# Kernel tuning notes

Hardware: AMD Instinct MI355X
Metric: run time of the kernel (lower is better)

Reference implementation:

```python
import jax, jax.numpy as jnp
import numpy as np

N = 25600      # nodes
DEG = 16       # incoming edges per node
E = N * DEG    # 409600 edges
B = 8          # graphs in batch
F = 7          # node features
H = 300        # hidden_channels
L = 100        # latent_channels


def _mlp(h, W1, b1, W2, b2, W3, b3):
    h = jax.nn.relu(h @ W1 + b1)
    h = jax.nn.relu(h @ W2 + b2)
    return h @ W3 + b3


def _edge_layer(x, src, dst, params):
    # PyG MessagePassing(aggr='max'), flow source_to_target:
    # x_j = x[src] (edge_index[0]), x_i = x[dst] (edge_index[1])
    x_i = x[dst]
    x_j = x[src]
    m = _mlp(jnp.concatenate([x_i, x_j - x_i], axis=-1), *params)  # [E, out]
    # every node has >=1 incoming edge by construction, so no empty segments
    return jax.ops.segment_max(m, dst, num_segments=x.shape[0])


def setup_inputs() -> dict:
    key = jax.random.key(0)
    ks = jax.random.split(key, 24)
    x = jax.random.normal(ks[0], (N, F), jnp.float32)
    dst = jnp.repeat(jnp.arange(N, dtype=jnp.int32), DEG)          # every node covered
    src = jax.random.randint(ks[1], (E,), 0, N, dtype=jnp.int32)
    edge_index = jnp.stack([src, dst])                              # [2, E]
    batch = jnp.repeat(jnp.arange(B, dtype=jnp.int32), N // B)     # sorted graph ids

    def lin(k, i, o):
        return jax.random.normal(k, (i, o), jnp.float32) / jnp.sqrt(jnp.float32(i))

    def bias(k, o):
        return jax.random.normal(k, (o,), jnp.float32) * 0.01

    inp = dict(x=x, edge_index=edge_index, batch=batch)
    # layer 0 MLP: 2*F -> H -> H -> L
    inp.update(l0_W1=lin(ks[2], 2 * F, H), l0_b1=bias(ks[3], H),
               l0_W2=lin(ks[4], H, H),     l0_b2=bias(ks[5], H),
               l0_W3=lin(ks[6], H, L),     l0_b3=bias(ks[7], L))
    # layer 1 MLP: 2*L -> H -> H -> L
    inp.update(l1_W1=lin(ks[8], 2 * L, H), l1_b1=bias(ks[9], H),
               l1_W2=lin(ks[10], H, H),    l1_b2=bias(ks[11], H),
               l1_W3=lin(ks[12], H, L),    l1_b3=bias(ks[13], L))
    # final lin: 3*L -> L -> L -> 1
    inp.update(lin_W1=lin(ks[14], 3 * L, L), lin_b1=bias(ks[15], L),
               lin_W2=lin(ks[16], L, L),     lin_b2=bias(ks[17], L),
               lin_W3=lin(ks[18], L, 1),     lin_b3=bias(ks[19], 1))
    return inp


def reference(x, edge_index, batch,
              l0_W1, l0_b1, l0_W2, l0_b2, l0_W3, l0_b3,
              l1_W1, l1_b1, l1_W2, l1_b2, l1_W3, l1_b3,
              lin_W1, lin_b1, lin_W2, lin_b2, lin_W3, lin_b3):
    src, dst = edge_index[0], edge_index[1]
    h = _edge_layer(x, src, dst, (l0_W1, l0_b1, l0_W2, l0_b2, l0_W3, l0_b3))
    h = jax.nn.relu(h)
    h = _edge_layer(h, src, dst, (l1_W1, l1_b1, l1_W2, l1_b2, l1_W3, l1_b3))
    h = jax.nn.relu(h)                                              # [N, L]
    addp = jax.ops.segment_sum(h, batch, num_segments=B)
    cnt = jax.ops.segment_sum(jnp.ones((h.shape[0], 1), h.dtype), batch, num_segments=B)
    meanp = addp / cnt
    maxp = jax.ops.segment_max(h, batch, num_segments=B)
    pooled = jnp.concatenate([addp, meanp, maxp], axis=1)           # [B, 3L]
    return _mlp(pooled, lin_W1, lin_b1, lin_W2, lin_b2, lin_W3, lin_b3)  # [B, 1]
```

## Files before the change

kernel.cpp:

```cpp
#include <hip/hip_runtime.h>

#define NNODES 25600
#define DEG 16
#define BGRAPHS 8
#define NPG (NNODES / BGRAPHS)
#define FDIM 7
#define HDIM 300
#define LDIM 100
#define HP 320
#define UVW 640
#define NT1 20
#define KS1 10
#define NT2 7
#define KS2 10
#define H0W 128
#define SSTR 328

typedef __attribute__((ext_vector_type(8))) _Float16 half8;
typedef __attribute__((ext_vector_type(2))) _Float16 half2v;
typedef __attribute__((ext_vector_type(4))) float floatx4;

__device__ __forceinline__ unsigned short f2h(float f) {
    _Float16 h = (_Float16)f;
    return __builtin_bit_cast(unsigned short, h);
}

union UV4H { uint4 v; half2v h[4]; };

__device__ __forceinline__ unsigned short packB(const float* W, int Kreal, int Nreal,
                                                int KS, int rel)
{
    int j = rel & 7, lane = (rel >> 3) & 63, rem = rel >> 9;
    int ks = rem % KS, nt = rem / KS;
    int k = ks * 32 + ((lane >> 4) << 3) + j;
    int n = nt * 16 + (lane & 15);
    float v = (k < Kreal && n < Nreal) ? W[k * Nreal + n] : 0.f;
    return f2h(v);
}

__device__ __forceinline__ unsigned short packProjW(const float* W1, int Ksub,
                                                    int KS, int rel)
{
    int j = rel & 7, lane = (rel >> 3) & 63, rem = rel >> 9;
    int ks = rem % KS, nt = rem / KS;
    int k = ks * 32 + ((lane >> 4) << 3) + j;
    int n = nt * 16 + (lane & 15);
    float v = 0.f;
    if (k < Ksub) {
        if (n < HP) { if (n < HDIM) v = W1[k * HDIM + n] - W1[(k + Ksub) * HDIM + n]; }
        else { int m = n - HP; if (m < HDIM) v = W1[(k + Ksub) * HDIM + m]; }
    }
    return f2h(v);
}

#define S0 102400
#define S1 102400
#define S2 35840
#define S3 35840
#define S4 81920
#define S5 20480
#define S6 1920
#define PACK_TOTAL (S0+S1+S2+S3+S4+S5+S6)

__global__ __launch_bounds__(256) void pack_all_kernel(
    const float* __restrict__ l0_W1, const float* __restrict__ l0_b1,
    const float* __restrict__ l0_W2, const float* __restrict__ l0_b2,
    const float* __restrict__ l0_W3,
    const float* __restrict__ l1_W1, const float* __restrict__ l1_b1,
    const float* __restrict__ l1_W2, const float* __restrict__ l1_b2,
    const float* __restrict__ l1_W3,
    unsigned short* __restrict__ PB2_0, unsigned short* __restrict__ PB2_1,
    unsigned short* __restrict__ PB3_0, unsigned short* __restrict__ PB3_1,
    unsigned short* __restrict__ PW1,  unsigned short* __restrict__ PW0,
    float* __restrict__ b2p_0, float* __restrict__ b2p_1,
    float* __restrict__ bp1,   float* __restrict__ bp0)
{
    int idx = blockIdx.x * 256 + threadIdx.x;
    if (idx >= PACK_TOTAL) return;
    if (idx < S0) { PB2_0[idx] = packB(l0_W2, HDIM, HDIM, KS1, idx); return; }
    idx -= S0;
    if (idx < S1) { PB2_1[idx] = packB(l1_W2, HDIM, HDIM, KS1, idx); return; }
    idx -= S1;
    if (idx < S2) { PB3_0[idx] = packB(l0_W3, HDIM, LDIM, KS2, idx); return; }
    idx -= S2;
    if (idx < S3) { PB3_1[idx] = packB(l1_W3, HDIM, LDIM, KS2, idx); return; }
    idx -= S3;
    if (idx < S4) { PW1[idx] = packProjW(l1_W1, LDIM, 4, idx); return; }
    idx -= S4;
    if (idx < S5) { PW0[idx] = packProjW(l0_W1, FDIM, 1, idx); return; }
    idx -= S5;
    if (idx < 320)       { b2p_0[idx] = (idx < HDIM) ? l0_b2[idx] : 0.f; return; }
    if (idx < 640)       { int n = idx - 320; b2p_1[n] = (n < HDIM) ? l1_b2[n] : 0.f; return; }
    if (idx < 1280)      { int n = idx - 640; bp1[n] = (n < HDIM) ? l1_b1[n] : 0.f; return; }
    { int n = idx - 1280; bp0[n] = (n < HDIM) ? l0_b1[n] : 0.f; }
}

template<int KS, bool A_IS_X>
__global__ __launch_bounds__(256) void proj_gemm_kernel(
    const void* __restrict__ Asrc, const unsigned short* __restrict__ PW,
    const float* __restrict__ bp,
    unsigned short* __restrict__ UV)
{
    __shared__ unsigned short As[4 * KS * 64 * 8];
    __shared__ unsigned short S[64 * SSTR];
    const int t = threadIdx.x;
    const int row0 = blockIdx.x * 64;

    if constexpr (A_IS_X) {
        const float* x = (const float*)Asrc;
        int lane = t & 63, mt = t >> 6;
        int quad = lane >> 4;
        int grow = row0 + mt * 16 + (lane & 15);
        unsigned short oz[8];
#pragma unroll
        for (int j = 0; j < 8; ++j) {
            int k = quad * 8 + j;
            oz[j] = (k < FDIM) ? f2h(x[grow * FDIM + k]) : (unsigned short)0;
        }
        *(uint4*)(As + t * 8) = *(uint4*)oz;
    } else {
        const unsigned short* h = (const unsigned short*)Asrc;
#pragma unroll
        for (int i = 0; i < 4; ++i) {
            int s = t + 256 * i;
            int lane = s & 63;
            int ks = (s >> 6) % KS;
            int mt = s / (KS * 64);
            int grow = row0 + mt * 16 + (lane & 15);
            int k0 = ks * 32 + ((lane >> 4) << 3);
            *(uint4*)(As + s * 8) = *(const uint4*)(h + (size_t)grow * H0W + k0);
        }
    }
    __syncthreads();

    const int w = t >> 6, lane = t & 63, quad = lane >> 4, l15 = lane & 15;

    for (int g = 0; g < 2; ++g) {
        const int ntb = g * 20 + w * 5;
        floatx4 c[5][4];
#pragma unroll
        for (int i = 0; i < 5; ++i)
#pragma unroll
            for (int mt = 0; mt < 4; ++mt) c[i][mt] = (floatx4){0.f, 0.f, 0.f, 0.f};
#pragma unroll
        for (int ks = 0; ks < KS; ++ks) {
            half8 a[4];
#pragma unroll
            for (int mt = 0; mt < 4; ++mt)
                a[mt] = *(const half8*)(As + ((mt * KS + ks) * 64 + lane) * 8);
#pragma unroll
            for (int i = 0; i < 5; ++i) {
                half8 b = *(const half8*)(PW + (size_t)(((ntb + i) * KS + ks) * 64 + lane) * 8);
#pragma unroll
                for (int mt = 0; mt < 4; ++mt)
                    c[i][mt] = __builtin_amdgcn_mfma_f32_16x16x32_f16(a[mt], b, c[i][mt], 0, 0, 0);
            }
        }
        __syncthreads();
#pragma unroll
        for (int i = 0; i < 5; ++i) {
            int colp = (w * 5 + i) * 16 + l15;
            float bb = bp[g * 320 + colp];
#pragma unroll
            for (int mt = 0; mt < 4; ++mt) {
#pragma unroll
                for (int r = 0; r < 4; ++r) {
                    int row = mt * 16 + quad * 4 + r;
                    S[row * SSTR + colp] = f2h(c[i][mt][r] + bb);
                }
            }
        }
        __syncthreads();
#pragma unroll
        for (int it = 0; it < 10; ++it) {
            int s = t + 256 * it;
            int row = s / 40, c4 = s - row * 40;
            uint4 v = *(const uint4*)(S + row * SSTR + c4 * 8);
            *(uint4*)(UV + (size_t)(row0 + row) * UVW + g * 320 + c4 * 8) = v;
        }
    }
}

template<bool OUT_HALF>
__global__ __launch_bounds__(512, 4) void edge_mfma_kernel(
    const unsigned short* __restrict__ UV,
    const int* __restrict__ src,
    const unsigned short* __restrict__ PB2, const float* __restrict__ b2p,
    const unsigned short* __restrict__ PB3, const float* __restrict__ b3,
    void* __restrict__ hout)
{
    __shared__ unsigned short Zs[4 * KS1 * 64 * 8];

    const int t = threadIdx.x;
    const int node0 = blockIdx.x * 4;
    const int lane = t & 63;
    const int w = t >> 6;
    const int quad = lane >> 4;
    const int l15 = lane & 15;
    const int slane = lane ^ ((lane & 0x30) >> 3);

    const int row16 = lane >> 2;
    const int part  = lane & 3;
    const int fl    = row16 + 16 * part;
    const int phys  = fl ^ (part << 1);

    const half2v hzero = {(_Float16)0.f, (_Float16)0.f};

#pragma unroll
    for (int i = 0; i < 5; ++i) {
        int s = t + 512 * i;
        int ks = (s >> 6) % KS1;
        int mt = s / (KS1 * 64);
        int m = mt * 16 + row16;
        int k0 = ks * 32 + part * 8;
        int srcn = src[node0 * 16 + m];
        UV4H ud, vd, o;
        ud.v = *(const uint4*)(UV + (size_t)(node0 + mt) * UVW + k0);
        vd.v = *(const uint4*)(UV + (size_t)srcn * UVW + HP + k0);
#pragma unroll
        for (int d = 0; d < 4; ++d) {
            half2v s2 = ud.h[d] + vd.h[d];
            o.h[d] = __builtin_elementwise_max(s2, hzero);
        }
        *(uint4*)(Zs + ((mt * KS1 + ks) * 64 + phys) * 8) = o.v;
    }
    __syncthreads();

    const int cnt1  = (w < 4) ? 3 : 2;
    const int base1 = (w < 4) ? 3 * w : 12 + 2 * (w - 4);
    floatx4 c1[3][4];
#pragma unroll
    for (int i = 0; i < 3; ++i)
#pragma unroll
        for (int mt = 0; mt < 4; ++mt) c1[i][mt] = (floatx4){0.f, 0.f, 0.f, 0.f};
    for (int ks = 0; ks < KS1; ++ks) {
        half8 a[4];
#pragma unroll
        for (int mt = 0; mt < 4; ++mt)
            a[mt] = *(const half8*)(Zs + ((mt * KS1 + ks) * 64 + slane) * 8);
#pragma unroll
        for (int i = 0; i < 3; ++i) {
            if (i < cnt1) {
                half8 b = *(const half8*)(PB2 + (size_t)(((base1 + i) * KS1 + ks) * 64 + lane) * 8);
#pragma unroll
                for (int mt = 0; mt < 4; ++mt)
                    c1[i][mt] = __builtin_amdgcn_mfma_f32_16x16x32_f16(a[mt], b, c1[i][mt], 0, 0, 0);
            }
        }
    }
    __syncthreads();

#pragma unroll
    for (int i = 0; i < 3; ++i) {
        if (i < cnt1) {
            int col = (base1 + i) * 16 + l15;
            float b2v = b2p[col];
            int slotbase = (col >> 5) * 64 + (((col >> 3) & 3) << 4) + quad * 4;
            int j = col & 7;
#pragma unroll
            for (int mt = 0; mt < 4; ++mt) {
#pragma unroll
                for (int r = 0; r < 4; ++r) {
                    float v = fmaxf(c1[i][mt][r] + b2v, 0.f);
                    Zs[(mt * KS1 * 64 + slotbase + r) * 8 + j] = f2h(v);
                }
            }
        }
    }
    __syncthreads();

    floatx4 c2[4];
#pragma unroll
    for (int mt = 0; mt < 4; ++mt) c2[mt] = (floatx4){0.f, 0.f, 0.f, 0.f};
    if (w < NT2) {
        for (int ks = 0; ks < KS2; ++ks) {
            half8 a[4];
#pragma unroll
            for (int mt = 0; mt < 4; ++mt)
                a[mt] = *(const half8*)(Zs + ((mt * KS2 + ks) * 64 + lane) * 8);
            half8 b = *(const half8*)(PB3 + (size_t)((w * KS2 + ks) * 64 + lane) * 8);
#pragma unroll
            for (int mt = 0; mt < 4; ++mt)
                c2[mt] = __builtin_amdgcn_mfma_f32_16x16x32_f16(a[mt], b, c2[mt], 0, 0, 0);
        }
    }

#pragma unroll
    for (int mt = 0; mt < 4; ++mt) {
        int node = node0 + mt;
        if (w < NT2) {
            int col = w * 16 + l15;
            floatx4 a = c2[mt];
            float mx = fmaxf(fmaxf(a[0], a[1]), fmaxf(a[2], a[3]));
            mx = fmaxf(mx, __shfl_xor(mx, 16, 64));
            mx = fmaxf(mx, __shfl_xor(mx, 32, 64));
            if (quad == 0) {
                if (OUT_HALF) {
                    unsigned short val = 0;
                    if (col < LDIM) val = f2h(fmaxf(mx + b3[col], 0.f));
                    ((unsigned short*)hout)[(size_t)node * H0W + col] = val;
                } else {
                    if (col < LDIM)
                        ((float*)hout)[(size_t)node * LDIM + col] = fmaxf(mx + b3[col], 0.f);
                }
            }
        }
        if (OUT_HALF && w == 7 && quad == 0)
            ((unsigned short*)hout)[(size_t)node * H0W + 112 + l15] = 0;
    }
}

__global__ __launch_bounds__(128) void pool1_kernel(
    const float* __restrict__ h, float* __restrict__ part)
{
    int g = blockIdx.x / 25;
    int sl = blockIdx.x % 25;
    int t = threadIdx.x;
    int base = g * NPG + sl * 128;
    if (t < LDIM) {
        float s = 0.f, mx = -1e30f;
        for (int i = 0; i < 128; ++i) {
            float v = h[(size_t)(base + i) * LDIM + t];
            s += v;
            mx = fmaxf(mx, v);
        }
        part[(size_t)blockIdx.x * 200 + t] = s;
        part[(size_t)blockIdx.x * 200 + 100 + t] = mx;
    }
}

__global__ __launch_bounds__(256) void final_kernel(
    const float* __restrict__ part,
    const float* __restrict__ W1, const float* __restrict__ b1,
    const float* __restrict__ W2, const float* __restrict__ b2,
    const float* __restrict__ W3, const float* __restrict__ b3,
    float* __restrict__ out)
{
    __shared__ float P[BGRAPHS][3 * LDIM];
    __shared__ float T1[BGRAPHS][LDIM];
    __shared__ float T2[BGRAPHS][LDIM];
    int t = threadIdx.x;
    for (int i = t; i < BGRAPHS * LDIM; i += 256) {
        int g = i / LDIM, f = i - (i / LDIM) * LDIM;
        float s = 0.f, mx = -1e30f;
        for (int sl = 0; sl < 25; ++sl) {
            s += part[(size_t)(g * 25 + sl) * 200 + f];
            mx = fmaxf(mx, part[(size_t)(g * 25 + sl) * 200 + 100 + f]);
        }
        P[g][f] = s;
        P[g][LDIM + f] = s * (1.0f / NPG);
        P[g][2 * LDIM + f] = mx;
    }
    __syncthreads();
    for (int i = t; i < BGRAPHS * LDIM; i += 256) {
        int g = i / LDIM, c = i - (i / LDIM) * LDIM;
        float a = b1[c];
        for (int k = 0; k < 3 * LDIM; ++k) a = fmaf(P[g][k], W1[k * LDIM + c], a);
        T1[g][c] = fmaxf(a, 0.f);
    }
    __syncthreads();
    for (int i = t; i < BGRAPHS * LDIM; i += 256) {
        int g = i / LDIM, c = i - (i / LDIM) * LDIM;
        float a = b2[c];
        for (int k = 0; k < LDIM; ++k) a = fmaf(T1[g][k], W2[k * LDIM + c], a);
        T2[g][c] = fmaxf(a, 0.f);
    }
    __syncthreads();
    if (t < BGRAPHS) {
        float a = b3[0];
        for (int k = 0; k < LDIM; ++k) a = fmaf(T2[t][k], W3[k], a);
        out[t] = a;
    }
}

extern "C" void kernel_launch(void* const* d_in, const int* in_sizes, int n_in,
                              void* d_out, int out_size, void* d_ws, size_t ws_size,
                              hipStream_t stream)
{
    const float* x      = (const float*)d_in[0];
    const int*   src    = (const int*)d_in[1];
    const float* l0_W1  = (const float*)d_in[3];
    const float* l0_b1  = (const float*)d_in[4];
    const float* l0_W2  = (const float*)d_in[5];
    const float* l0_b2  = (const float*)d_in[6];
    const float* l0_W3  = (const float*)d_in[7];
    const float* l0_b3  = (const float*)d_in[8];
    const float* l1_W1  = (const float*)d_in[9];
    const float* l1_b1  = (const float*)d_in[10];
    const float* l1_W2  = (const float*)d_in[11];
    const float* l1_b2  = (const float*)d_in[12];
    const float* l1_W3  = (const float*)d_in[13];
    const float* l1_b3  = (const float*)d_in[14];
    const float* lin_W1 = (const float*)d_in[15];
    const float* lin_b1 = (const float*)d_in[16];
    const float* lin_W2 = (const float*)d_in[17];
    const float* lin_b2 = (const float*)d_in[18];
    const float* lin_W3 = (const float*)d_in[19];
    const float* lin_b3 = (const float*)d_in[20];
    float* out = (float*)d_out;

    char* p = (char*)d_ws;
    unsigned short* UV    = (unsigned short*)p;  p += (size_t)NNODES * UVW * 2;
    unsigned short* h0b   = (unsigned short*)p;  p += (size_t)NNODES * H0W * 2;
    float* h1             = (float*)p;           p += (size_t)NNODES * LDIM * 4;
    unsigned short* PB2_0 = (unsigned short*)p;  p += (size_t)S0 * 2;
    unsigned short* PB2_1 = (unsigned short*)p;  p += (size_t)S1 * 2;
    unsigned short* PB3_0 = (unsigned short*)p;  p += (size_t)S2 * 2;
    unsigned short* PB3_1 = (unsigned short*)p;  p += (size_t)S3 * 2;
    unsigned short* PW1   = (unsigned short*)p;  p += (size_t)S4 * 2;
    unsigned short* PW0   = (unsigned short*)p;  p += (size_t)S5 * 2;
    float* b2p_0          = (float*)p;           p += HP * 4;
    float* b2p_1          = (float*)p;           p += HP * 4;
    float* bp1            = (float*)p;           p += 640 * 4;
    float* bp0            = (float*)p;           p += 640 * 4;
    float* part           = (float*)p;           p += (size_t)200 * 200 * 4;

    pack_all_kernel<<<(PACK_TOTAL + 255) / 256, 256, 0, stream>>>(
        l0_W1, l0_b1, l0_W2, l0_b2, l0_W3,
        l1_W1, l1_b1, l1_W2, l1_b2, l1_W3,
        PB2_0, PB2_1, PB3_0, PB3_1, PW1, PW0, b2p_0, b2p_1, bp1, bp0);

    proj_gemm_kernel<1, true><<<NNODES / 64, 256, 0, stream>>>(x, PW0, bp0, UV);
    edge_mfma_kernel<true><<<NNODES / 4, 512, 0, stream>>>(UV, src, PB2_0, b2p_0, PB3_0, l0_b3, h0b);
    proj_gemm_kernel<4, false><<<NNODES / 64, 256, 0, stream>>>(h0b, PW1, bp1, UV);
    edge_mfma_kernel<false><<<NNODES / 4, 512, 0, stream>>>(UV, src, PB2_1, b2p_1, PB3_1, l1_b3, h1);
    pool1_kernel<<<200, 128, 0, stream>>>(h1, part);
    final_kernel<<<1, 256, 0, stream>>>(part, lin_W1, lin_b1, lin_W2, lin_b2, lin_W3, lin_b3, out);
}
```

Before: 439.5 us.

## Retile edge MFMA warps into 2x4 M-by-N grid for balanced work

Warps now split the work as two row groups (node tiles) by four column groups, instead of each warp covering all four node tiles for a slice of columns. Each warp loads fewer A fragments from shared memory and reuses each B fragment across two node tiles. Both GEMMs now keep all eight warps busy, where before the second GEMM had an idle warp and the first had uneven 3/2 column counts. In exchange, B weight fragments are now read twice per block from global/L2, and the loops are partly unrolled, which may raise register pressure.

New measurement: 480.5 us. +9.3%, slower.

```diff
diff --git a/kernel.cpp b/kernel.cpp
--- a/kernel.cpp
+++ b/kernel.cpp
@@ -195,6 +195,8 @@
     const int node0 = blockIdx.x * 4;
     const int lane = t & 63;
     const int w = t >> 6;
+    const int mw = w & 1;
+    const int nw = w >> 1;
     const int quad = lane >> 4;
     const int l15 = lane & 15;
     const int slane = lane ^ ((lane & 0x30) >> 3);
@@ -226,86 +228,92 @@
     }
     __syncthreads();
 
-    const int cnt1  = (w < 4) ? 3 : 2;
-    const int base1 = (w < 4) ? 3 * w : 12 + 2 * (w - 4);
-    floatx4 c1[3][4];
-#pragma unroll
-    for (int i = 0; i < 3; ++i)
-#pragma unroll
-        for (int mt = 0; mt < 4; ++mt) c1[i][mt] = (floatx4){0.f, 0.f, 0.f, 0.f};
+    floatx4 c1[5][2];
+#pragma unroll
+    for (int i = 0; i < 5; ++i)
+#pragma unroll
+        for (int mtl = 0; mtl < 2; ++mtl) c1[i][mtl] = (floatx4){0.f, 0.f, 0.f, 0.f};
+#pragma unroll 2
     for (int ks = 0; ks < KS1; ++ks) {
-        half8 a[4];
-#pragma unroll
-        for (int mt = 0; mt < 4; ++mt)
-            a[mt] = *(const half8*)(Zs + ((mt * KS1 + ks) * 64 + slane) * 8);
-#pragma unroll
-        for (int i = 0; i < 3; ++i) {
-            if (i < cnt1) {
-                half8 b = *(const half8*)(PB2 + (size_t)(((base1 + i) * KS1 + ks) * 64 + lane) * 8);
-#pragma unroll
-                for (int mt = 0; mt < 4; ++mt)
-                    c1[i][mt] = __builtin_amdgcn_mfma_f32_16x16x32_f16(a[mt], b, c1[i][mt], 0, 0, 0);
+        half8 a[2];
+#pragma unroll
+        for (int mtl = 0; mtl < 2; ++mtl)
+            a[mtl] = *(const half8*)(Zs + (((2 * mw + mtl) * KS1 + ks) * 64 + slane) * 8);
+#pragma unroll
+        for (int i = 0; i < 5; ++i) {
+            half8 b = *(const half8*)(PB2 + (size_t)(((nw * 5 + i) * KS1 + ks) * 64 + lane) * 8);
+#pragma unroll
+            for (int mtl = 0; mtl < 2; ++mtl)
+                c1[i][mtl] = __builtin_amdgcn_mfma_f32_16x16x32_f16(a[mtl], b, c1[i][mtl], 0, 0, 0);
+        }
+    }
+    __syncthreads();
+
+#pragma unroll
+    for (int i = 0; i < 5; ++i) {
+        int col = (nw * 5 + i) * 16 + l15;
+        float b2v = b2p[col];
+        int slotbase = (col >> 5) * 64 + (((col >> 3) & 3) << 4) + quad * 4;
+        int j = col & 7;
+#pragma unroll
+        for (int mtl = 0; mtl < 2; ++mtl) {
+            int mt = 2 * mw + mtl;
+#pragma unroll
+            for (int r = 0; r < 4; ++r) {
+                float v = fmaxf(c1[i][mtl][r] + b2v, 0.f);
+                Zs[(mt * KS1 * 64 + slotbase + r) * 8 + j] = f2h(v);
             }
         }
     }
     __syncthreads();
 
-#pragma unroll
-    for (int i = 0; i < 3; ++i) {
-        if (i < cnt1) {
-            int col = (base1 + i) * 16 + l15;
-            float b2v = b2p[col];
-            int slotbase = (col >> 5) * 64 + (((col >> 3) & 3) << 4) + quad * 4;
-            int j = col & 7;
-#pragma unroll
-            for (int mt = 0; mt < 4; ++mt) {
-#pragma unroll
-                for (int r = 0; r < 4; ++r) {
-                    float v = fmaxf(c1[i][mt][r] + b2v, 0.f);
-                    Zs[(mt * KS1 * 64 + slotbase + r) * 8 + j] = f2h(v);
+    const int cnt2 = (nw < 3) ? 2 : 1;
+    floatx4 c2[2][2];
+#pragma unroll
+    for (int i = 0; i < 2; ++i)
+#pragma unroll
+        for (int mtl = 0; mtl < 2; ++mtl) c2[i][mtl] = (floatx4){0.f, 0.f, 0.f, 0.f};
+#pragma unroll 2
+    for (int ks = 0; ks < KS2; ++ks) {
+        half8 a[2];
+#pragma unroll
+        for (int mtl = 0; mtl < 2; ++mtl)
+            a[mtl] = *(const half8*)(Zs + (((2 * mw + mtl) * KS2 + ks) * 64 + lane) * 8);
+#pragma unroll
+        for (int i = 0; i < 2; ++i) {
+            if (i < cnt2) {
+                half8 b = *(const half8*)(PB3 + (size_t)(((nw * 2 + i) * KS2 + ks) * 64 + lane) * 8);
+#pragma unroll
+                for (int mtl = 0; mtl < 2; ++mtl)
+                    c2[i][mtl] = __builtin_amdgcn_mfma_f32_16x16x32_f16(a[mtl], b, c2[i][mtl], 0, 0, 0);
+            }
+        }
+    }
+
+#pragma unroll
+    for (int mtl = 0; mtl < 2; ++mtl) {
+        int node = node0 + 2 * mw + mtl;
+#pragma unroll
+        for (int i = 0; i < 2; ++i) {
+            if (i < cnt2) {
+                int col = (nw * 2 + i) * 16 + l15;
+                floatx4 a = c2[i][mtl];
+                float mx = fmaxf(fmaxf(a[0], a[1]), fmaxf(a[2], a[3]));
+                mx = fmaxf(mx, __shfl_xor(mx, 16, 64));
+                mx = fmaxf(mx, __shfl_xor(mx, 32, 64));
+                if (quad == 0) {
+                    if (OUT_HALF) {
+                        unsigned short val = 0;
+                        if (col < LDIM) val = f2h(fmaxf(mx + b3[col], 0.f));
+                        ((unsigned short*)hout)[(size_t)node * H0W + col] = val;
+                    } else {
+                        if (col < LDIM)
+                            ((float*)hout)[(size_t)node * LDIM + col] = fmaxf(mx + b3[col], 0.f);
+                    }
                 }
             }
         }
-    }
-    __syncthreads();
-
-    floatx4 c2[4];
-#pragma unroll
-    for (int mt = 0; mt < 4; ++mt) c2[mt] = (floatx4){0.f, 0.f, 0.f, 0.f};
-    if (w < NT2) {
-        for (int ks = 0; ks < KS2; ++ks) {
-            half8 a[4];
-#pragma unroll
-            for (int mt = 0; mt < 4; ++mt)
-                a[mt] = *(const half8*)(Zs + ((mt * KS2 + ks) * 64 + lane) * 8);
-            half8 b = *(const half8*)(PB3 + (size_t)((w * KS2 + ks) * 64 + lane) * 8);
-#pragma unroll
-            for (int mt = 0; mt < 4; ++mt)
-                c2[mt] = __builtin_amdgcn_mfma_f32_16x16x32_f16(a[mt], b, c2[mt], 0, 0, 0);
-        }
-    }
-
-#pragma unroll
-    for (int mt = 0; mt < 4; ++mt) {
-        int node = node0 + mt;
-        if (w < NT2) {
-            int col = w * 16 + l15;
-            floatx4 a = c2[mt];
-            float mx = fmaxf(fmaxf(a[0], a[1]), fmaxf(a[2], a[3]));
-            mx = fmaxf(mx, __shfl_xor(mx, 16, 64));
-            mx = fmaxf(mx, __shfl_xor(mx, 32, 64));
-            if (quad == 0) {
-                if (OUT_HALF) {
-                    unsigned short val = 0;
-                    if (col < LDIM) val = f2h(fmaxf(mx + b3[col], 0.f));
-                    ((unsigned short*)hout)[(size_t)node * H0W + col] = val;
-                } else {
-                    if (col < LDIM)
-                        ((float*)hout)[(size_t)node * LDIM + col] = fmaxf(mx + b3[col], 0.f);
-                }
-            }
-        }
-        if (OUT_HALF && w == 7 && quad == 0)
+        if (OUT_HALF && nw == 3 && quad == 0)
             ((unsigned short*)hout)[(size_t)node * H0W + 112 + l15] = 0;
     }
 }
```
